# Optimization experiments

Measured on AMD Instinct MI355X. Metric: run time of the kernel, lower is better.

## Reference

```python
import jax, jax.numpy as jnp
import numpy as np

N_NODES = 100000
N_EDGES = 3200000
DIMS = [3, 64, 64, 64, 128, 1024, 512, 256, 2]  # per GCNemb.__init__


def setup_inputs() -> dict:
    key = jax.random.key(0)
    ks = jax.random.split(key, 2 + 2 * 8)
    x = jax.random.normal(ks[0], (N_NODES, DIMS[0]), dtype=jnp.float32)
    edge_index = jax.random.randint(ks[1], (2, N_EDGES), 0, N_NODES, dtype=jnp.int64)
    inp = {"x": x, "edge_index": edge_index}
    for i in range(8):
        scale = 1.0 / np.sqrt(DIMS[i])
        inp[f"W{i}"] = jax.random.normal(ks[2 + 2 * i], (DIMS[i], DIMS[i + 1]), dtype=jnp.float32) * scale
        inp[f"b{i}"] = jnp.zeros((DIMS[i + 1],), dtype=jnp.float32)
    return inp


def _gcn_norm(edge_index, n):
    # PyG GCNConv default: add self-loops, symmetric normalization.
    loop = jnp.arange(n, dtype=edge_index.dtype)
    row = jnp.concatenate([edge_index[0], loop])  # source
    col = jnp.concatenate([edge_index[1], loop])  # target
    deg = jax.ops.segment_sum(jnp.ones_like(col, dtype=jnp.float32), col, num_segments=n)
    dinv = jnp.where(deg > 0, jax.lax.rsqrt(deg), 0.0)
    norm = dinv[row] * dinv[col]  # [E+N]
    return row, col, norm


def _gcn_conv(x, W, b, row, col, norm, n):
    h = x @ W  # [N, out]
    agg = jax.ops.segment_sum(h[row] * norm[:, None], col, num_segments=n)
    return agg + b


def reference(x, edge_index, W0, b0, W1, b1, W2, b2, W3, b3, W4, b4, W5, b5, W6, b6, W7, b7):
    n = x.shape[0]
    row, col, norm = _gcn_norm(edge_index, n)
    Ws = [W0, W1, W2, W3, W4, W5, W6, W7]
    bs = [b0, b1, b2, b3, b4, b5, b6, b7]
    for i in range(7):
        x = jax.nn.relu(_gcn_conv(x, Ws[i], bs[i], row, col, norm, n))
    return _gcn_conv(x, Ws[7], bs[7], row, col, norm, n)
```

## Files before the change

### kernel.cpp

```cpp
#include <hip/hip_runtime.h>
#include <hip/hip_bf16.h>
#include <cstdint>
#include <cstddef>


#define TPB 256

typedef short short8 __attribute__((ext_vector_type(8)));
typedef float f32x4 __attribute__((ext_vector_type(4)));

__device__ __forceinline__ float b2f(unsigned short u) {
    union { unsigned int i; float f; } c; c.i = ((unsigned int)u) << 16; return c.f;
}
__device__ __forceinline__ unsigned short f2b(float f) {
    __hip_bfloat16 h = __float2bfloat16(f);
    union { __hip_bfloat16 h; unsigned short u; } c; c.h = h; return c.u;
}

__device__ __forceinline__ void async_copy16(void* lds, const void* g) {
    __builtin_amdgcn_global_load_lds(
        (const __attribute__((address_space(1))) void*)g,
        (__attribute__((address_space(3))) void*)lds,
        16, 0, 0);
}


__global__ void count_deg_kernel(const int* __restrict__ col, int* __restrict__ deg,
                                 int E, int n) {
    int e = blockIdx.x * blockDim.x + threadIdx.x;
    if (e < E) {
        int c = col[e];
        if ((unsigned)c < (unsigned)n) atomicAdd(&deg[c], 1);
    }
}

__global__ void dinv_kernel(const int* __restrict__ deg, float* __restrict__ dinv, int n) {
    int i = blockIdx.x * blockDim.x + threadIdx.x;
    if (i < n) dinv[i] = 1.0f / sqrtf((float)(deg[i] + 1));
}

__global__ void scan_kernel(const int* __restrict__ deg, int* __restrict__ rowptr,
                            int* __restrict__ cursor, int n) {
    __shared__ int sums[1024];
    int tid = threadIdx.x;
    int chunk = (n + 1023) >> 10;
    int lo = tid * chunk;
    int hi = lo + chunk; if (hi > n) hi = n;
    int s = 0;
    for (int i = lo; i < hi; i++) s += deg[i];
    sums[tid] = s;
    __syncthreads();
    for (int off = 1; off < 1024; off <<= 1) {
        int v = (tid >= off) ? sums[tid - off] : 0;
        __syncthreads();
        sums[tid] += v;
        __syncthreads();
    }
    int run = (tid == 0) ? 0 : sums[tid - 1];
    for (int i = lo; i < hi; i++) {
        rowptr[i] = run; cursor[i] = run;
        run += deg[i];
    }
    if (tid == 1023) rowptr[n] = sums[1023];
}

__global__ void fill_csr_kernel(const int* __restrict__ row, const int* __restrict__ col,
                                int* __restrict__ cursor, int* __restrict__ srcs,
                                int E, int n) {
    int e = blockIdx.x * blockDim.x + threadIdx.x;
    if (e < E) {
        int c = col[e];
        if ((unsigned)c < (unsigned)n) {
            int pos = atomicAdd(&cursor[c], 1);
            if ((unsigned)pos < (unsigned)E) srcs[pos] = row[e];
        }
    }
}

__global__ void convert_wt_kernel(const float* __restrict__ W, unsigned short* __restrict__ Wt,
                                  int K, int M) {
    int idx = blockIdx.x * blockDim.x + threadIdx.x;
    if (idx < K * M) {
        int k = idx / M, m = idx % M;
        Wt[(size_t)m * K + k] = f2b(W[idx]);
    }
}


template <int VEC> struct Pack;
template <> struct Pack<1> { using T = unsigned short; };
template <> struct Pack<2> { using T = unsigned int; };
template <> struct Pack<4> { using T = uint2; };
template <> struct Pack<8> { using T = uint4; };

template <int VEC>
__global__ __launch_bounds__(TPB) void agg_bf16_kernel(
        const unsigned short* __restrict__ x, unsigned short* __restrict__ out,
        const int* __restrict__ rowptr, const int* __restrict__ srcs,
        const float* __restrict__ dinv, const float* __restrict__ bias,
        int n, int relu) {
    using P = typename Pack<VEC>::T;
    const int d = 64 * VEC;
    int wid  = (blockIdx.x * blockDim.x + threadIdx.x) >> 6;
    int lane = threadIdx.x & 63;
    if (wid >= n) return;
    int start = rowptr[wid], end = rowptr[wid + 1];
    float acc0[VEC], acc1[VEC], acc2[VEC], acc3[VEC];
#pragma unroll
    for (int j = 0; j < VEC; j++) { acc0[j] = 0.f; acc1[j] = 0.f; acc2[j] = 0.f; acc3[j] = 0.f; }
    const int fo = lane * VEC;
    union U { P v; unsigned short u[VEC]; };

    for (int base = start; base < end; base += 64) {
        int idx = base + lane;
        int clamped = (idx < end) ? idx : (end - 1);
        int sv = srcs[clamped];
        float dv = 0.f;
        if (idx < end) dv = dinv[sv];
        int cnt = end - base; if (cnt > 64) cnt = 64;
        int j = 0;
        for (; j + 4 <= cnt; j += 4) {
            int   s0 = __shfl(sv, j),     s1 = __shfl(sv, j + 1);
            int   s2 = __shfl(sv, j + 2), s3 = __shfl(sv, j + 3);
            float e0 = __shfl(dv, j),     e1 = __shfl(dv, j + 1);
            float e2 = __shfl(dv, j + 2), e3 = __shfl(dv, j + 3);
            U l0, l1, l2, l3;
            l0.v = *(const P*)(x + (size_t)s0 * d + fo);
            l1.v = *(const P*)(x + (size_t)s1 * d + fo);
            l2.v = *(const P*)(x + (size_t)s2 * d + fo);
            l3.v = *(const P*)(x + (size_t)s3 * d + fo);
#pragma unroll
            for (int q = 0; q < VEC; q++) {
                acc0[q] = fmaf(e0, b2f(l0.u[q]), acc0[q]);
                acc1[q] = fmaf(e1, b2f(l1.u[q]), acc1[q]);
                acc2[q] = fmaf(e2, b2f(l2.u[q]), acc2[q]);
                acc3[q] = fmaf(e3, b2f(l3.u[q]), acc3[q]);
            }
        }
        for (; j < cnt; j++) {
            int   s0 = __shfl(sv, j);
            float e0 = __shfl(dv, j);
            U l0; l0.v = *(const P*)(x + (size_t)s0 * d + fo);
#pragma unroll
            for (int q = 0; q < VEC; q++) acc0[q] = fmaf(e0, b2f(l0.u[q]), acc0[q]);
        }
    }

    float di = dinv[wid];
    U ls; ls.v = *(const P*)(x + (size_t)wid * d + fo);
    U st;
#pragma unroll
    for (int j = 0; j < VEC; j++) {
        float a = (acc0[j] + acc1[j]) + (acc2[j] + acc3[j]);
        float v = di * (a + di * b2f(ls.u[j]));
        if (bias) v += bias[fo + j];
        if (relu) v = fmaxf(v, 0.f);
        st.u[j] = f2b(v);
    }
    *(P*)(out + (size_t)wid * d + fo) = st.v;
}

template <int D, int FUSE64>
__global__ __launch_bounds__(TPB) void agg_small_wave_kernel(
        const float* __restrict__ x, float* __restrict__ outf,
        unsigned short* __restrict__ outb,
        const int* __restrict__ rowptr, const int* __restrict__ srcs,
        const float* __restrict__ dinv, const float* __restrict__ bias,
        const float* __restrict__ W, int n, int relu) {
    int wid  = (blockIdx.x * blockDim.x + threadIdx.x) >> 6;
    int lane = threadIdx.x & 63;
    if (wid >= n) return;
    int start = rowptr[wid], end = rowptr[wid + 1];
    float acc[D];
#pragma unroll
    for (int j = 0; j < D; j++) acc[j] = 0.f;
    for (int e = start + lane; e < end; e += 64) {
        int s = srcs[e];
        float ds = dinv[s];
#pragma unroll
        for (int j = 0; j < D; j++) acc[j] = fmaf(ds, x[(size_t)s * D + j], acc[j]);
    }
#pragma unroll
    for (int j = 0; j < D; j++) {
#pragma unroll
        for (int off = 32; off >= 1; off >>= 1) acc[j] += __shfl_xor(acc[j], off);
    }
    float di = dinv[wid];
    float aggv[D];
#pragma unroll
    for (int j = 0; j < D; j++) aggv[j] = di * (acc[j] + di * x[(size_t)wid * D + j]);

    if (FUSE64) {
        float v = bias[lane];
#pragma unroll
        for (int j = 0; j < D; j++) v = fmaf(aggv[j], W[j * 64 + lane], v);
        v = fmaxf(v, 0.f);
        outb[(size_t)wid * 64 + lane] = f2b(v);
    } else {
        if (lane < D) {
            float v = aggv[lane];
            if (bias) v += bias[lane];
            if (relu) v = fmaxf(v, 0.f);
            outf[(size_t)wid * D + lane] = v;
        }
    }
}

__global__ __launch_bounds__(TPB) void gemm_dot2_kernel(
        const unsigned short* __restrict__ A, const float* __restrict__ W,
        float* __restrict__ pre, int n) {
    int wid  = (blockIdx.x * blockDim.x + threadIdx.x) >> 6;
    int lane = threadIdx.x & 63;
    if (wid >= n) return;
    union { uint2 v; unsigned short u[4]; } a;
    a.v = *(const uint2*)(A + (size_t)wid * 256 + lane * 4);
    float c0 = 0.f, c1 = 0.f;
#pragma unroll
    for (int j = 0; j < 4; j++) {
        float av = b2f(a.u[j]);
        c0 = fmaf(av, W[(lane * 4 + j) * 2 + 0], c0);
        c1 = fmaf(av, W[(lane * 4 + j) * 2 + 1], c1);
    }
#pragma unroll
    for (int off = 32; off >= 1; off >>= 1) {
        c0 += __shfl_xor(c0, off);
        c1 += __shfl_xor(c1, off);
    }
    if (lane == 0) { pre[(size_t)wid * 2 + 0] = c0; pre[(size_t)wid * 2 + 1] = c1; }
}

__device__ inline float to_f(float v) { return v; }
__device__ inline float to_f(__hip_bfloat16 v) { return __bfloat162float(v); }
__device__ inline void from_f(float v, float& d) { d = v; }
__device__ inline void from_f(float v, __hip_bfloat16& d) { d = __float2bfloat16(v); }

#define BM 64
#define BN 64
#define BK 16
template <typename TA, typename TC>
__global__ __launch_bounds__(256) void gemm_valu_kernel(
        const TA* __restrict__ A, const float* __restrict__ W,
        const float* __restrict__ bias, TC* __restrict__ C,
        int nr, int K, int M, int relu, int addbias) {
    __shared__ float As[BK][BM + 4];
    __shared__ float Bs[BK][BN + 4];
    int tid  = threadIdx.x;
    int row0 = blockIdx.x * BM;
    int col0 = blockIdx.y * BN;
    int rm = (tid >> 4) << 2;
    int rn = (tid & 15) << 2;
    float acc[4][4];
#pragma unroll
    for (int y = 0; y < 4; y++)
#pragma unroll
        for (int xj = 0; xj < 4; xj++) acc[y][xj] = 0.f;

    for (int kk = 0; kk < K; kk += BK) {
#pragma unroll
        for (int i = 0; i < 4; i++) {
            int idx = tid + i * 256;
            int k = idx & 15, r = idx >> 4;
            int gr = row0 + r, gk = kk + k;
            float v = 0.f;
            if (gr < nr && gk < K) v = to_f(A[(size_t)gr * K + gk]);
            As[k][r] = v;
        }
#pragma unroll
        for (int i = 0; i < 4; i++) {
            int idx = tid + i * 256;
            int k = idx >> 6, c = idx & 63;
            int gk = kk + k, gc = col0 + c;
            float v = 0.f;
            if (gk < K && gc < M) v = W[(size_t)gk * M + gc];
            Bs[k][c] = v;
        }
        __syncthreads();
#pragma unroll
        for (int k = 0; k < BK; k++) {
            float a[4], b[4];
#pragma unroll
            for (int j = 0; j < 4; j++) { a[j] = As[k][rm + j]; b[j] = Bs[k][rn + j]; }
#pragma unroll
            for (int y = 0; y < 4; y++)
#pragma unroll
                for (int xj = 0; xj < 4; xj++)
                    acc[y][xj] = fmaf(a[y], b[xj], acc[y][xj]);
        }
        __syncthreads();
    }
#pragma unroll
    for (int y = 0; y < 4; y++) {
        int gr = row0 + rm + y;
        if (gr >= nr) continue;
#pragma unroll
        for (int xj = 0; xj < 4; xj++) {
            int gc = col0 + rn + xj;
            if (gc >= M) continue;
            float v = acc[y][xj];
            if (addbias) v += bias[gc];
            if (relu) v = fmaxf(v, 0.f);
            from_f(v, C[(size_t)gr * M + gc]);
        }
    }
}

template <typename TA, typename TC>
static inline void launch_gemm_valu(const TA* A, const float* W, const float* bias,
                                    TC* C, int nr, int K, int M, int relu, int addbias,
                                    hipStream_t stream) {
    dim3 grid((nr + BM - 1) / BM, (M + BN - 1) / BN);
    gemm_valu_kernel<TA, TC><<<grid, 256, 0, stream>>>(A, W, bias, C, nr, K, M, relu, addbias);
}

__global__ __launch_bounds__(256) void gemm_mfma_kernel(
        const unsigned short* __restrict__ A, const unsigned short* __restrict__ Wt,
        const float* __restrict__ bias, unsigned short* __restrict__ C,
        int nr, int K, int M, int relu, int addbias) {
    __shared__ alignas(16) short As[128 * 32];
    __shared__ alignas(16) short Bs[128 * 32];
    const int tid  = threadIdx.x;
    const int w    = tid >> 6;
    const int lane = tid & 63;
    const int wr   = w >> 1;
    const int wc   = w & 1;
    const int row0 = blockIdx.x * 128;
    const int col0 = blockIdx.y * 128;

    f32x4 acc[4][4];
#pragma unroll
    for (int i = 0; i < 4; i++)
#pragma unroll
        for (int j = 0; j < 4; j++) acc[i][j] = {0.f, 0.f, 0.f, 0.f};

    const int lrow   = lane >> 2;
    const int lcolB  = (lane & 3) * 16;
    const int fm     = lane & 15;
    const int fq     = lane >> 4;

    for (int kk = 0; kk < K; kk += 32) {
#pragma unroll
        for (int i = 0; i < 2; i++) {
            int r = w * 32 + i * 16 + lrow;
            int grow = row0 + r;
            const char* g = (const char*)A + ((size_t)grow * K + kk) * 2 + lcolB;
            short* lds = &As[(w * 32 + i * 16) * 32];
            if (grow < nr) async_copy16(lds, g);
        }
#pragma unroll
        for (int i = 0; i < 2; i++) {
            int r = w * 32 + i * 16 + lrow;
            int gcol = col0 + r;
            const char* g = (const char*)Wt + ((size_t)gcol * K + kk) * 2 + lcolB;
            short* lds = &Bs[(w * 32 + i * 16) * 32];
            async_copy16(lds, g);
        }
        __syncthreads();

        short8 a[4], b[4];
#pragma unroll
        for (int i = 0; i < 4; i++) {
            a[i] = *(const short8*)&As[(wr * 64 + i * 16 + fm) * 32 + fq * 8];
            b[i] = *(const short8*)&Bs[(wc * 64 + i * 16 + fm) * 32 + fq * 8];
        }
#pragma unroll
        for (int mi = 0; mi < 4; mi++)
#pragma unroll
            for (int ni = 0; ni < 4; ni++)
                acc[mi][ni] = __builtin_amdgcn_mfma_f32_16x16x32_bf16(
                    a[mi], b[ni], acc[mi][ni], 0, 0, 0);
        __syncthreads();
    }

#pragma unroll
    for (int mi = 0; mi < 4; mi++) {
#pragma unroll
        for (int r = 0; r < 4; r++) {
            int row = row0 + wr * 64 + mi * 16 + fq * 4 + r;
            if (row >= nr) continue;
            size_t rb = (size_t)row * M;
#pragma unroll
            for (int ni = 0; ni < 4; ni++) {
                int col = col0 + wc * 64 + ni * 16 + fm;
                float v = acc[mi][ni][r];
                if (addbias) v += bias[col];
                if (relu) v = fmaxf(v, 0.f);
                C[rb + col] = f2b(v);
            }
        }
    }
}

static inline void launch_gemm_mfma(const unsigned short* A, const unsigned short* Wt,
                                    const float* bias, unsigned short* C,
                                    int nr, int K, int M, int relu, int addbias,
                                    hipStream_t stream) {
    dim3 grid((nr + 127) / 128, M / 128);
    gemm_mfma_kernel<<<grid, 256, 0, stream>>>(A, Wt, bias, C, nr, K, M, relu, addbias);
}


static inline size_t al256(size_t x) { return (x + 255) & ~(size_t)255; }

extern "C" void kernel_launch(void* const* d_in, const int* in_sizes, int n_in,
                              void* d_out, int out_size, void* d_ws, size_t ws_size,
                              hipStream_t stream) {
    const float* x  = (const float*)d_in[0];
    const int*   ei = (const int*)d_in[1];
    const int E = in_sizes[1] / 2;
    const int n = in_sizes[0] / 3;
    const int* rowv = ei;
    const int* colv = ei + E;

    const float* Wf[8]; const float* bt[8];
    for (int i = 0; i < 8; i++) { Wf[i] = (const float*)d_in[2 + 2 * i]; bt[i] = (const float*)d_in[3 + 2 * i]; }

    char* p = (char*)d_ws;
    size_t used = 0;
    auto carve = [&](size_t bytes) -> char* {
        char* r = p + used; used += al256(bytes); return r;
    };
    int*   deg    = (int*)carve((size_t)n * 4);
    float* dinv   = (float*)carve((size_t)n * 4);
    int*   rowptr = (int*)carve((size_t)(n + 1) * 4);
    int*   cursor = (int*)carve((size_t)(n + 1) * 4);
    int*   srcs   = (int*)carve((size_t)E * 4);
    unsigned short* bufA = (unsigned short*)carve((size_t)n * 512 * 2);
    unsigned short* bufB = (unsigned short*)carve((size_t)n * 512 * 2);
    const size_t wt3e = 64 * 128, wt4e = 128 * 1024, wt5e = 1024 * 512, wt6e = 512 * 256;
    unsigned short* wt3 = (unsigned short*)carve((wt3e + wt4e + wt5e + wt6e) * 2);
    unsigned short* wt4 = wt3 + wt3e;
    unsigned short* wt5 = wt4 + wt4e;
    unsigned short* wt6 = wt5 + wt5e;
    size_t avail = (ws_size > used) ? (ws_size - used) : 0;
    int chunk = (int)(avail / (1024 * 2));
    if (chunk > n) chunk = n;
    chunk &= ~127;
    if (chunk < 2048) chunk = 2048;
    char* tmp_raw = carve((size_t)chunk * 1024 * 2);
    unsigned short* tmpb = (unsigned short*)tmp_raw;
    float* tmpf = (float*)tmp_raw;

    const int EB = (E + TPB - 1) / TPB;
    const int NB = (n + TPB - 1) / TPB;
    const int NW = (n + 3) / 4;

    hipMemsetAsync(deg, 0, (size_t)n * 4, stream);
    count_deg_kernel<<<EB, TPB, 0, stream>>>(colv, deg, E, n);
    dinv_kernel<<<NB, TPB, 0, stream>>>(deg, dinv, n);
    scan_kernel<<<1, 1024, 0, stream>>>(deg, rowptr, cursor, n);
    fill_csr_kernel<<<EB, TPB, 0, stream>>>(rowv, colv, cursor, srcs, E, n);

    convert_wt_kernel<<<(int)((wt3e + 255) / 256), 256, 0, stream>>>(Wf[3], wt3, 64, 128);
    convert_wt_kernel<<<(int)((wt4e + 255) / 256), 256, 0, stream>>>(Wf[4], wt4, 128, 1024);
    convert_wt_kernel<<<(int)((wt5e + 255) / 256), 256, 0, stream>>>(Wf[5], wt5, 1024, 512);
    convert_wt_kernel<<<(int)((wt6e + 255) / 256), 256, 0, stream>>>(Wf[6], wt6, 512, 256);

    agg_small_wave_kernel<3, 1><<<NW, TPB, 0, stream>>>(
        x, nullptr, bufA, rowptr, srcs, dinv, bt[0], Wf[0], n, 1);

    agg_bf16_kernel<1><<<NW, TPB, 0, stream>>>(bufA, bufB, rowptr, srcs, dinv, nullptr, n, 0);
    launch_gemm_valu<__hip_bfloat16, __hip_bfloat16>((const __hip_bfloat16*)bufB, Wf[1], bt[1],
                                                     (__hip_bfloat16*)bufA, n, 64, 64, 1, 1, stream);
    agg_bf16_kernel<1><<<NW, TPB, 0, stream>>>(bufA, bufB, rowptr, srcs, dinv, nullptr, n, 0);
    launch_gemm_valu<__hip_bfloat16, __hip_bfloat16>((const __hip_bfloat16*)bufB, Wf[2], bt[2],
                                                     (__hip_bfloat16*)bufA, n, 64, 64, 1, 1, stream);

    agg_bf16_kernel<1><<<NW, TPB, 0, stream>>>(bufA, bufB, rowptr, srcs, dinv, nullptr, n, 0);
    launch_gemm_mfma(bufB, wt3, bt[3], bufA, n, 64, 128, 1, 1, stream);

    agg_bf16_kernel<2><<<NW, TPB, 0, stream>>>(bufA, bufB, rowptr, srcs, dinv, nullptr, n, 0);
    for (int r0 = 0; r0 < n; r0 += chunk) {
        int ch = n - r0; if (ch > chunk) ch = chunk;
        launch_gemm_mfma(bufB + (size_t)r0 * 128, wt4, bt[4], tmpb, ch, 128, 1024, 1, 1, stream);
        launch_gemm_mfma(tmpb, wt5, nullptr, bufA + (size_t)r0 * 512, ch, 1024, 512, 0, 0, stream);
    }
    agg_bf16_kernel<8><<<NW, TPB, 0, stream>>>(bufA, bufB, rowptr, srcs, dinv, bt[5], n, 1);

    launch_gemm_mfma(bufB, wt6, nullptr, bufA, n, 512, 256, 0, 0, stream);
    agg_bf16_kernel<4><<<NW, TPB, 0, stream>>>(bufA, bufB, rowptr, srcs, dinv, bt[6], n, 1);

    gemm_dot2_kernel<<<NW, TPB, 0, stream>>>(bufB, Wf[7], tmpf, n);
    agg_small_wave_kernel<2, 0><<<NW, TPB, 0, stream>>>(
        tmpf, (float*)d_out, nullptr, rowptr, srcs, dinv, bt[7], nullptr, n, 0);
}
```

Baseline: 2.347 ms.

## Pack source index with dinv into CSR edges and split wide aggregation into column windows

New measurement: 2.221 ms. 1.06x faster.

```diff
diff --git a/kernel.cpp b/kernel.cpp
--- a/kernel.cpp
+++ b/kernel.cpp
@@ -65,14 +65,18 @@
 }
 
 __global__ void fill_csr_kernel(const int* __restrict__ row, const int* __restrict__ col,
-                                int* __restrict__ cursor, int* __restrict__ srcs,
+                                const float* __restrict__ dinv,
+                                int* __restrict__ cursor, int2* __restrict__ es,
                                 int E, int n) {
     int e = blockIdx.x * blockDim.x + threadIdx.x;
     if (e < E) {
         int c = col[e];
         if ((unsigned)c < (unsigned)n) {
+            int r = row[e];
             int pos = atomicAdd(&cursor[c], 1);
-            if ((unsigned)pos < (unsigned)E) srcs[pos] = row[e];
+            if ((unsigned)pos < (unsigned)E) {
+                es[pos] = make_int2(r, __float_as_int(dinv[r]));
+            }
         }
     }
 }
@@ -91,16 +95,14 @@
 template <> struct Pack<1> { using T = unsigned short; };
 template <> struct Pack<2> { using T = unsigned int; };
 template <> struct Pack<4> { using T = uint2; };
-template <> struct Pack<8> { using T = uint4; };
 
 template <int VEC>
-__global__ __launch_bounds__(TPB) void agg_bf16_kernel(
+__global__ __launch_bounds__(TPB) void agg_win_kernel(
         const unsigned short* __restrict__ x, unsigned short* __restrict__ out,
-        const int* __restrict__ rowptr, const int* __restrict__ srcs,
+        const int* __restrict__ rowptr, const int2* __restrict__ es,
         const float* __restrict__ dinv, const float* __restrict__ bias,
-        int n, int relu) {
+        int n, int d, int wb, int relu) {
     using P = typename Pack<VEC>::T;
-    const int d = 64 * VEC;
     int wid  = (blockIdx.x * blockDim.x + threadIdx.x) >> 6;
     int lane = threadIdx.x & 63;
     if (wid >= n) return;
@@ -108,15 +110,15 @@
     float acc0[VEC], acc1[VEC], acc2[VEC], acc3[VEC];
 #pragma unroll
     for (int j = 0; j < VEC; j++) { acc0[j] = 0.f; acc1[j] = 0.f; acc2[j] = 0.f; acc3[j] = 0.f; }
-    const int fo = lane * VEC;
+    const int fo = wb + lane * VEC;
     union U { P v; unsigned short u[VEC]; };
 
     for (int base = start; base < end; base += 64) {
         int idx = base + lane;
         int clamped = (idx < end) ? idx : (end - 1);
-        int sv = srcs[clamped];
-        float dv = 0.f;
-        if (idx < end) dv = dinv[sv];
+        int2 ev = es[clamped];
+        int   sv = ev.x;
+        float dv = (idx < end) ? __int_as_float(ev.y) : 0.f;
         int cnt = end - base; if (cnt > 64) cnt = 64;
         int j = 0;
         for (; j + 4 <= cnt; j += 4) {
@@ -164,7 +166,7 @@
 __global__ __launch_bounds__(TPB) void agg_small_wave_kernel(
         const float* __restrict__ x, float* __restrict__ outf,
         unsigned short* __restrict__ outb,
-        const int* __restrict__ rowptr, const int* __restrict__ srcs,
+        const int* __restrict__ rowptr, const int2* __restrict__ es,
         const float* __restrict__ dinv, const float* __restrict__ bias,
         const float* __restrict__ W, int n, int relu) {
     int wid  = (blockIdx.x * blockDim.x + threadIdx.x) >> 6;
@@ -175,8 +177,9 @@
 #pragma unroll
     for (int j = 0; j < D; j++) acc[j] = 0.f;
     for (int e = start + lane; e < end; e += 64) {
-        int s = srcs[e];
-        float ds = dinv[s];
+        int2 ev = es[e];
+        int s = ev.x;
+        float ds = __int_as_float(ev.y);
 #pragma unroll
         for (int j = 0; j < D; j++) acc[j] = fmaf(ds, x[(size_t)s * D + j], acc[j]);
     }
@@ -423,7 +426,7 @@
     float* dinv   = (float*)carve((size_t)n * 4);
     int*   rowptr = (int*)carve((size_t)(n + 1) * 4);
     int*   cursor = (int*)carve((size_t)(n + 1) * 4);
-    int*   srcs   = (int*)carve((size_t)E * 4);
+    int2*  es     = (int2*)carve((size_t)E * 8);
     unsigned short* bufA = (unsigned short*)carve((size_t)n * 512 * 2);
     unsigned short* bufB = (unsigned short*)carve((size_t)n * 512 * 2);
     const size_t wt3e = 64 * 128, wt4e = 128 * 1024, wt5e = 1024 * 512, wt6e = 512 * 256;
@@ -448,7 +451,7 @@
     count_deg_kernel<<<EB, TPB, 0, stream>>>(colv, deg, E, n);
     dinv_kernel<<<NB, TPB, 0, stream>>>(deg, dinv, n);
     scan_kernel<<<1, 1024, 0, stream>>>(deg, rowptr, cursor, n);
-    fill_csr_kernel<<<EB, TPB, 0, stream>>>(rowv, colv, cursor, srcs, E, n);
+    fill_csr_kernel<<<EB, TPB, 0, stream>>>(rowv, colv, dinv, cursor, es, E, n);
 
     convert_wt_kernel<<<(int)((wt3e + 255) / 256), 256, 0, stream>>>(Wf[3], wt3, 64, 128);
     convert_wt_kernel<<<(int)((wt4e + 255) / 256), 256, 0, stream>>>(Wf[4], wt4, 128, 1024);
@@ -456,30 +459,31 @@
     convert_wt_kernel<<<(int)((wt6e + 255) / 256), 256, 0, stream>>>(Wf[6], wt6, 512, 256);
 
     agg_small_wave_kernel<3, 1><<<NW, TPB, 0, stream>>>(
-        x, nullptr, bufA, rowptr, srcs, dinv, bt[0], Wf[0], n, 1);
-
-    agg_bf16_kernel<1><<<NW, TPB, 0, stream>>>(bufA, bufB, rowptr, srcs, dinv, nullptr, n, 0);
+        x, nullptr, bufA, rowptr, es, dinv, bt[0], Wf[0], n, 1);
+
+    agg_win_kernel<1><<<NW, TPB, 0, stream>>>(bufA, bufB, rowptr, es, dinv, nullptr, n, 64, 0, 0);
     launch_gemm_valu<__hip_bfloat16, __hip_bfloat16>((const __hip_bfloat16*)bufB, Wf[1], bt[1],
                                                      (__hip_bfloat16*)bufA, n, 64, 64, 1, 1, stream);
-    agg_bf16_kernel<1><<<NW, TPB, 0, stream>>>(bufA, bufB, rowptr, srcs, dinv, nullptr, n, 0);
+    agg_win_kernel<1><<<NW, TPB, 0, stream>>>(bufA, bufB, rowptr, es, dinv, nullptr, n, 64, 0, 0);
     launch_gemm_valu<__hip_bfloat16, __hip_bfloat16>((const __hip_bfloat16*)bufB, Wf[2], bt[2],
                                                      (__hip_bfloat16*)bufA, n, 64, 64, 1, 1, stream);
 
-    agg_bf16_kernel<1><<<NW, TPB, 0, stream>>>(bufA, bufB, rowptr, srcs, dinv, nullptr, n, 0);
+    agg_win_kernel<1><<<NW, TPB, 0, stream>>>(bufA, bufB, rowptr, es, dinv, nullptr, n, 64, 0, 0);
     launch_gemm_mfma(bufB, wt3, bt[3], bufA, n, 64, 128, 1, 1, stream);
 
-    agg_bf16_kernel<2><<<NW, TPB, 0, stream>>>(bufA, bufB, rowptr, srcs, dinv, nullptr, n, 0);
+    agg_win_kernel<2><<<NW, TPB, 0, stream>>>(bufA, bufB, rowptr, es, dinv, nullptr, n, 128, 0, 0);
     for (int r0 = 0; r0 < n; r0 += chunk) {
         int ch = n - r0; if (ch > chunk) ch = chunk;
         launch_gemm_mfma(bufB + (size_t)r0 * 128, wt4, bt[4], tmpb, ch, 128, 1024, 1, 1, stream);
         launch_gemm_mfma(tmpb, wt5, nullptr, bufA + (size_t)r0 * 512, ch, 1024, 512, 0, 0, stream);
     }
-    agg_bf16_kernel<8><<<NW, TPB, 0, stream>>>(bufA, bufB, rowptr, srcs, dinv, bt[5], n, 1);
+    agg_win_kernel<4><<<NW, TPB, 0, stream>>>(bufA, bufB, rowptr, es, dinv, bt[5], n, 512, 0, 1);
+    agg_win_kernel<4><<<NW, TPB, 0, stream>>>(bufA, bufB, rowptr, es, dinv, bt[5], n, 512, 256, 1);
 
     launch_gemm_mfma(bufB, wt6, nullptr, bufA, n, 512, 256, 0, 0, stream);
-    agg_bf16_kernel<4><<<NW, TPB, 0, stream>>>(bufA, bufB, rowptr, srcs, dinv, bt[6], n, 1);
+    agg_win_kernel<4><<<NW, TPB, 0, stream>>>(bufA, bufB, rowptr, es, dinv, bt[6], n, 256, 0, 1);
 
     gemm_dot2_kernel<<<NW, TPB, 0, stream>>>(bufB, Wf[7], tmpf, n);
     agg_small_wave_kernel<2, 0><<<NW, TPB, 0, stream>>>(
-        tmpf, (float*)d_out, nullptr, rowptr, srcs, dinv, bt[7], nullptr, n, 0);
-}
+        tmpf, (float*)d_out, nullptr, rowptr, es, dinv, bt[7], nullptr, n, 0);
+}
```
